# Kernel optimization log

Hardware: AMD Instinct MI355X
Metric: run time of the kernel (lower is better)

## Reference

```python
import jax, jax.numpy as jnp
from jax import lax
import numpy as np

B, T, D, U, K = 32, 1000, 512, 5, 3  # batch, frames, idim, upsample_times, conv kernel (l_order+r_order+1)
THRESHOLD = 1.0
TAIL = 0.45


def setup_inputs() -> dict:
    key = jax.random.key(0)
    ks = jax.random.split(key, 6)
    return {
        "encoder_out": jax.random.normal(ks[0], (B, T, D), jnp.float32),
        "mask": jnp.ones((B, 1, T), jnp.float32),
        "conv_w": jax.random.normal(ks[1], (D, D, K), jnp.float32) * 0.02,  # torch Conv1d [out,in,k]
        "conv_b": jnp.zeros((D,), jnp.float32),
        "up_w": jax.random.normal(ks[2], (D, D, U), jnp.float32) * 0.02,    # torch ConvTranspose1d [in,out,k]
        "up_b": jnp.zeros((D,), jnp.float32),
        "w1": jax.random.normal(ks[3], (D,), jnp.float32) * 0.05,           # cif_output Linear(D,1)
        "b1": jnp.zeros((), jnp.float32),
        "w2": jax.random.normal(ks[4], (D,), jnp.float32) * 0.05,           # cif_output2 Linear(D,1)
        "b2": jnp.zeros((), jnp.float32),
    }


def _cif(hidden, alphas, threshold):
    # hidden: [B, Tt, D], alphas: [B, Tt]
    Bb, Tt, Dd = hidden.shape

    def step(carry, inp):
        integrate, frame = carry
        alpha, h_t = inp  # [B], [B, D]
        dist_completion = 1.0 - integrate
        integrate = integrate + alpha
        fires_t = integrate
        fire = integrate >= threshold
        integrate = jnp.where(fire, integrate - 1.0, integrate)
        cur = jnp.where(fire, dist_completion, alpha)
        frame_out = frame + cur[:, None] * h_t
        frame = jnp.where(fire[:, None], (alpha - cur)[:, None] * h_t, frame_out)
        return (integrate, frame), (fires_t, frame_out)

    init = (jnp.zeros((Bb,), hidden.dtype), jnp.zeros((Bb, Dd), hidden.dtype))
    _, (fires, frames) = lax.scan(step, init, (alphas.T, jnp.swapaxes(hidden, 0, 1)))
    fires = fires.T                      # [B, Tt]
    frames = jnp.swapaxes(frames, 0, 1)  # [B, Tt, D]

    fire_mask = fires >= threshold

    def gather_b(frames_b, mask_b):
        pos = jnp.cumsum(mask_b.astype(jnp.int32)) - 1
        pos = jnp.where(mask_b, pos, Tt)  # non-fires -> out of range, dropped
        return jnp.zeros((Tt, Dd), frames_b.dtype).at[pos].set(frames_b, mode='drop')

    acoustic = jax.vmap(gather_b)(frames, fire_mask)  # [B, Tt, D] zero-padded
    return acoustic, fires


def reference(encoder_out, mask, conv_w, conv_b, up_w, up_b, w1, b1, w2, b2):
    Bb, Tt, Dd = encoder_out.shape
    context = jnp.swapaxes(encoder_out, 1, 2)           # [B, D, T]
    queries = jnp.pad(context, ((0, 0), (0, 0), (1, 1)))  # ConstantPad1d((1,1))
    conv = lax.conv_general_dilated(queries, conv_w, (1,), 'VALID',
                                    dimension_numbers=('NCH', 'OIH', 'NCH'))
    output = jax.nn.relu(conv + conv_b[None, :, None])  # [B, D, T]

    # ConvTranspose1d(stride=kernel=U, pad=0): non-overlapping -> einsum
    out2 = jnp.einsum('bit,ioj->btjo', output, up_w).reshape(Bb, Tt * U, Dd) + up_b  # [B, T*U, D]
    alphas2 = jax.nn.relu(jax.nn.sigmoid(out2 @ w2 + b2) * 1.0 - 0.0)  # smooth_factor2=1, noise_threshold2=0
    mask2 = jnp.swapaxes(jnp.broadcast_to(mask, (Bb, U, Tt)), 1, 2).reshape(Bb, Tt * U)
    alphas2 = alphas2 * mask2
    token_num2 = alphas2.sum(-1)

    h1 = jnp.swapaxes(output, 1, 2)  # [B, T, D]
    alphas = jax.nn.relu(jax.nn.sigmoid(h1 @ w1 + b1) * 1.0 - 0.0)  # smooth_factor=1, noise_threshold=0
    maskT = jnp.swapaxes(mask, 1, 2)[..., 0]  # [B, T]
    alphas = alphas * maskT

    # tail_process_fn (tail_threshold=0.45, mask given)
    zeros_t = jnp.zeros((Bb, 1), alphas.dtype)
    ones_t = jnp.ones((Bb, 1), alphas.dtype)
    mask_1 = jnp.concatenate([maskT, zeros_t], axis=1)
    mask_2 = jnp.concatenate([ones_t, maskT], axis=1)
    tail_add = (mask_2 - mask_1) * TAIL
    alphas_t = jnp.concatenate([alphas, zeros_t], axis=1) + tail_add  # [B, T+1]
    hidden = jnp.concatenate([encoder_out, jnp.zeros((Bb, 1, Dd), encoder_out.dtype)], axis=1)
    token_num = jnp.floor(alphas_t.sum(-1))

    acoustic_embeds, cif_peak = _cif(hidden, alphas_t, THRESHOLD)
    return acoustic_embeds, token_num, alphas_t, cif_peak, token_num2
```

## Files before the change

### kernel.cpp

```cpp
#include <hip/hip_runtime.h>
#include <math.h>

#define TB 32
#define TT 1000
#define TD 512
#define TU 5
#define TT1 1001

#define OFF_ACC  0
#define OFF_TOKN 16400384
#define OFF_ALPH 16400416
#define OFF_PEAK 16432448
#define OFF_TOK2 16464480

typedef _Float16 half8 __attribute__((ext_vector_type(8)));
typedef _Float16 half2t __attribute__((ext_vector_type(2)));
typedef float float4t __attribute__((ext_vector_type(4)));

typedef __attribute__((address_space(3))) uint32_t lds_u32_t;
typedef __attribute__((address_space(1))) const uint32_t g_u32_t;
#define GLOAD_LDS(gp, lp) __builtin_amdgcn_global_load_lds((g_u32_t*)(gp), (lds_u32_t*)(lp), 16, 0, 0)

#define BSTR 72
#define ASTR 200
#define EROWS 1032

#define WS_ARAW1 0
#define WS_ARAW2 32000
#define WS_VMAT  192000
#define WS_C2    194560
#define WS_WA    194564
#define WS_WB    226596
#define WS_FIRE  258628
#define WS_NF    290660
#define WS_ENCS_BYTES 1163264ull
#define WS_CWS_BYTES  (WS_ENCS_BYTES + 76059648ull)
#define WS_NEED_BYTES (WS_CWS_BYTES + 3276800ull)

__global__ __launch_bounds__(256) void kzero(float* araw1, float* araw2, float* tok2) {
    int idx = blockIdx.x * 256 + threadIdx.x;
    int stride = gridDim.x * 256;
    for (int i = idx; i < TB * TT; i += stride) araw1[i] = 0.f;
    for (int i = idx; i < TB * TT * TU; i += stride) araw2[i] = 0.f;
    if (idx < TB) tok2[idx] = 0.f;
}

__global__ __launch_bounds__(256) void kc2(const float* __restrict__ up_b, const float* __restrict__ w2,
                                           const float* __restrict__ b2, float* __restrict__ c2out) {
    int tid = threadIdx.x;
    float p = 0.f;
    for (int o = tid; o < TD; o += 256) p += up_b[o] * w2[o];
#pragma unroll
    for (int m = 1; m < 64; m <<= 1) p += __shfl_xor(p, m);
    __shared__ float wsum[4];
    if ((tid & 63) == 0) wsum[tid >> 6] = p;
    __syncthreads();
    if (tid == 0) c2out[0] = b2[0] + wsum[0] + wsum[1] + wsum[2] + wsum[3];
}

__global__ __launch_bounds__(64) void kv(const float* __restrict__ up_w, const float* __restrict__ w2,
                                         float* __restrict__ vmat) {
    int i = blockIdx.x, lane = threadIdx.x;
    float s0 = 0, s1 = 0, s2 = 0, s3 = 0, s4 = 0;
    for (int o = lane; o < TD; o += 64) {
        float w = w2[o];
        const float* p = up_w + (size_t)i * (TD * TU) + o * TU;
        s0 += p[0] * w; s1 += p[1] * w; s2 += p[2] * w; s3 += p[3] * w; s4 += p[4] * w;
    }
#pragma unroll
    for (int m = 1; m < 64; m <<= 1) {
        s0 += __shfl_xor(s0, m); s1 += __shfl_xor(s1, m); s2 += __shfl_xor(s2, m);
        s3 += __shfl_xor(s3, m); s4 += __shfl_xor(s4, m);
    }
    if (lane == 0) {
        float* d = vmat + i * TU;
        d[0] = s0; d[1] = s1; d[2] = s2; d[3] = s3; d[4] = s4;
    }
}

__global__ __launch_bounds__(256) void ksplitE(const float* __restrict__ enc, _Float16* __restrict__ encs) {
    int t = blockIdx.x, b = blockIdx.y, tid = threadIdx.x;
    int c = tid * 2;
    const float* p = &enc[((size_t)b * TT + t) * TD + c];
    float x0 = p[0], x1 = p[1];
    _Float16 h0 = (_Float16)x0, h1 = (_Float16)x1;
    _Float16 l0 = (_Float16)(x0 - (float)h0), l1 = (_Float16)(x1 - (float)h1);
    int ic = c >> 5, pos = c & 31;
    size_t base = ((size_t)(b * 16 + ic) * EROWS + 1 + t) * BSTR + pos;
    encs[base] = h0; encs[base + 1] = h1;
    encs[base + 32] = l0; encs[base + 33] = l1;
}

__global__ __launch_bounds__(256) void kpad(_Float16* __restrict__ encs) {
    uint32_t* p = (uint32_t*)encs;
    int idx = blockIdx.x * 256 + threadIdx.x;
    int stride = gridDim.x * 256;
    const int total = 512 * 32 * 36;
    for (int u = idx; u < total; u += stride) {
        int bic = u / (32 * 36);
        int r = (u / 36) % 32;
        int w = u % 36;
        int row = (r == 0) ? 0 : 1000 + r;
        p[((size_t)bic * EROWS + row) * 36 + w] = 0u;
    }
}

__global__ __launch_bounds__(64) void ksplitW(const float* __restrict__ cw, _Float16* __restrict__ cws) {
    int o = blockIdx.x, lane = threadIdx.x;
    for (int u = lane; u < 16 * 32 * 3; u += 64) {
        int tap = u % 3, pos = (u / 3) % 32, ic = u / 96;
        float x = cw[((size_t)o * TD + ic * 32 + pos) * 3 + tap];
        _Float16 h = (_Float16)x;
        _Float16 l = (_Float16)(x - (float)h);
        size_t base = (((size_t)(o >> 5) * 16 + ic) * 32 + (o & 31)) * ASTR + tap * 64;
        cws[base + pos] = h;
        cws[base + 32 + pos] = l;
    }
}

__global__ __launch_bounds__(256, 2) void kconvMD(const _Float16* __restrict__ encs,
                                                  const _Float16* __restrict__ cws,
                                                  const float* __restrict__ cb, const float* __restrict__ w1,
                                                  const float* __restrict__ vmat,
                                                  float* __restrict__ araw1, float* __restrict__ araw2) {
    __shared__ _Float16 sB[258 * BSTR];
    __shared__ _Float16 sA[64 * ASTR];

    const int tid = threadIdx.x;
    const int t0 = blockIdx.x * 256;
    const int oc = blockIdx.y;
    const int b = blockIdx.z;
    const int o0 = oc * 64;
    const int wv = tid >> 6, lane = tid & 63;
    const int q = lane >> 4, l15 = lane & 15;

    float4t acc[4][4];
#pragma unroll
    for (int i = 0; i < 4; ++i)
#pragma unroll
        for (int j = 0; j < 4; ++j) acc[i][j] = (float4t){0.f, 0.f, 0.f, 0.f};

    for (int ic = 0; ic < 16; ++ic) {
        __syncthreads();
        const _Float16* gB = encs + ((size_t)(b * 16 + ic) * EROWS + t0) * BSTR;
        for (int c = tid; c < 2322; c += 256) GLOAD_LDS(gB + c * 8, &sB[c * 8]);
        const _Float16* gA0 = cws + ((size_t)((oc * 2 + 0) * 16 + ic) * 32) * ASTR;
        const _Float16* gA1 = cws + ((size_t)((oc * 2 + 1) * 16 + ic) * 32) * ASTR;
        for (int c = tid; c < 800; c += 256) GLOAD_LDS(gA0 + c * 8, &sA[c * 8]);
        for (int c = tid; c < 800; c += 256) GLOAD_LDS(gA1 + c * 8, &sA[6400 + c * 8]);
        __syncthreads();
#pragma unroll
        for (int tap = 0; tap < 3; ++tap) {
            half8 Bh[4], Bl[4];
#pragma unroll
            for (int tt = 0; tt < 4; ++tt) {
                int s = wv * 64 + tt * 16 + l15 + tap;
                Bh[tt] = *(const half8*)&sB[s * BSTR + q * 8];
                Bl[tt] = *(const half8*)&sB[s * BSTR + 32 + q * 8];
            }
#pragma unroll
            for (int ot = 0; ot < 4; ++ot) {
                const int orow = ot * 16 + l15;
                half8 Ah = *(const half8*)&sA[orow * ASTR + tap * 64 + q * 8];
                half8 Al = *(const half8*)&sA[orow * ASTR + tap * 64 + 32 + q * 8];
#pragma unroll
                for (int tt = 0; tt < 4; ++tt) {
                    acc[ot][tt] = __builtin_amdgcn_mfma_f32_16x16x32_f16(Ah, Bh[tt], acc[ot][tt], 0, 0, 0);
                    acc[ot][tt] = __builtin_amdgcn_mfma_f32_16x16x32_f16(Ah, Bl[tt], acc[ot][tt], 0, 0, 0);
                    acc[ot][tt] = __builtin_amdgcn_mfma_f32_16x16x32_f16(Al, Bh[tt], acc[ot][tt], 0, 0, 0);
                }
            }
        }
    }

#pragma unroll
    for (int tt = 0; tt < 4; ++tt) {
        int t = t0 + wv * 64 + tt * 16 + l15;
        float s1 = 0.f, sa = 0.f, sb = 0.f, sc = 0.f, sd = 0.f, se = 0.f;
#pragma unroll
        for (int ot = 0; ot < 4; ++ot) {
#pragma unroll
            for (int r = 0; r < 4; ++r) {
                int o = o0 + ot * 16 + q * 4 + r;
                float rv = fmaxf(acc[ot][tt][r] + cb[o], 0.f);
                s1 = fmaf(w1[o], rv, s1);
                const float* vp = &vmat[o * 5];
                sa = fmaf(vp[0], rv, sa); sb = fmaf(vp[1], rv, sb);
                sc = fmaf(vp[2], rv, sc); sd = fmaf(vp[3], rv, sd);
                se = fmaf(vp[4], rv, se);
            }
        }
        s1 += __shfl_xor(s1, 16); sa += __shfl_xor(sa, 16); sb += __shfl_xor(sb, 16);
        sc += __shfl_xor(sc, 16); sd += __shfl_xor(sd, 16); se += __shfl_xor(se, 16);
        s1 += __shfl_xor(s1, 32); sa += __shfl_xor(sa, 32); sb += __shfl_xor(sb, 32);
        sc += __shfl_xor(sc, 32); sd += __shfl_xor(sd, 32); se += __shfl_xor(se, 32);
        if (q == 0 && t < TT) {
            atomicAdd(&araw1[b * TT + t], s1);
            float* p2 = &araw2[(b * TT + t) * 5];
            atomicAdd(p2 + 0, sa); atomicAdd(p2 + 1, sb); atomicAdd(p2 + 2, sc);
            atomicAdd(p2 + 3, sd); atomicAdd(p2 + 4, se);
        }
    }
}

__global__ __launch_bounds__(256, 3) void kconvM(const float* __restrict__ enc, const float* __restrict__ cw,
                                                 const float* __restrict__ cb, const float* __restrict__ w1,
                                                 const float* __restrict__ vmat,
                                                 float* __restrict__ araw1, float* __restrict__ araw2) {
    __shared__ _Float16 sB[258 * BSTR];
    __shared__ _Float16 sA[32 * ASTR];

    const int tid = threadIdx.x;
    const int t0 = blockIdx.x * 256;
    const int o0 = blockIdx.y * 32;
    const int b = blockIdx.z;
    const int wv = tid >> 6, lane = tid & 63;
    const int q = lane >> 4, l15 = lane & 15;

    float4t acc[2][4];
#pragma unroll
    for (int i = 0; i < 2; ++i)
#pragma unroll
        for (int j = 0; j < 4; ++j) acc[i][j] = (float4t){0.f, 0.f, 0.f, 0.f};

    for (int i0 = 0; i0 < TD; i0 += 32) {
        __syncthreads();
        for (int u = tid; u < 258 * 16; u += 256) {
            int s = u >> 4, ii2 = (u & 15) << 1;
            int t = t0 - 1 + s;
            float x0 = 0.f, x1 = 0.f;
            if (t >= 0 && t < TT) {
                const float* p = &enc[((size_t)b * TT + t) * TD + i0 + ii2];
                x0 = p[0]; x1 = p[1];
            }
            _Float16 h0 = (_Float16)x0, h1 = (_Float16)x1;
            _Float16 l0 = (_Float16)(x0 - (float)h0), l1 = (_Float16)(x1 - (float)h1);
            half2t hh; hh[0] = h0; hh[1] = h1;
            half2t ll; ll[0] = l0; ll[1] = l1;
            *(half2t*)&sB[s * BSTR + ii2] = hh;
            *(half2t*)&sB[s * BSTR + 32 + ii2] = ll;
        }
        for (int u = tid; u < 32 * 16; u += 256) {
            int o = u >> 4, ii2 = (u & 15) << 1;
            const float* p = &cw[((size_t)(o0 + o) * TD + i0 + ii2) * 3];
#pragma unroll
            for (int k = 0; k < 3; ++k) {
                float x0 = p[k], x1 = p[3 + k];
                _Float16 h0 = (_Float16)x0, h1 = (_Float16)x1;
                _Float16 l0 = (_Float16)(x0 - (float)h0), l1 = (_Float16)(x1 - (float)h1);
                half2t hh; hh[0] = h0; hh[1] = h1;
                half2t ll; ll[0] = l0; ll[1] = l1;
                *(half2t*)&sA[o * ASTR + k * 64 + ii2] = hh;
                *(half2t*)&sA[o * ASTR + k * 64 + 32 + ii2] = ll;
            }
        }
        __syncthreads();
#pragma unroll
        for (int tap = 0; tap < 3; ++tap) {
            half8 Bh[4], Bl[4];
#pragma unroll
            for (int tt = 0; tt < 4; ++tt) {
                int s = wv * 64 + tt * 16 + l15 + tap;
                Bh[tt] = *(const half8*)&sB[s * BSTR + q * 8];
                Bl[tt] = *(const half8*)&sB[s * BSTR + 32 + q * 8];
            }
#pragma unroll
            for (int ot = 0; ot < 2; ++ot) {
                const int orow = ot * 16 + l15;
                half8 Ah = *(const half8*)&sA[orow * ASTR + tap * 64 + q * 8];
                half8 Al = *(const half8*)&sA[orow * ASTR + tap * 64 + 32 + q * 8];
#pragma unroll
                for (int tt = 0; tt < 4; ++tt) {
                    acc[ot][tt] = __builtin_amdgcn_mfma_f32_16x16x32_f16(Ah, Bh[tt], acc[ot][tt], 0, 0, 0);
                    acc[ot][tt] = __builtin_amdgcn_mfma_f32_16x16x32_f16(Ah, Bl[tt], acc[ot][tt], 0, 0, 0);
                    acc[ot][tt] = __builtin_amdgcn_mfma_f32_16x16x32_f16(Al, Bh[tt], acc[ot][tt], 0, 0, 0);
                }
            }
        }
    }

#pragma unroll
    for (int tt = 0; tt < 4; ++tt) {
        int t = t0 + wv * 64 + tt * 16 + l15;
        float s1 = 0.f, sa = 0.f, sb = 0.f, sc = 0.f, sd = 0.f, se = 0.f;
#pragma unroll
        for (int ot = 0; ot < 2; ++ot) {
#pragma unroll
            for (int r = 0; r < 4; ++r) {
                int o = o0 + ot * 16 + q * 4 + r;
                float rv = fmaxf(acc[ot][tt][r] + cb[o], 0.f);
                s1 = fmaf(w1[o], rv, s1);
                const float* vp = &vmat[o * 5];
                sa = fmaf(vp[0], rv, sa); sb = fmaf(vp[1], rv, sb);
                sc = fmaf(vp[2], rv, sc); sd = fmaf(vp[3], rv, sd);
                se = fmaf(vp[4], rv, se);
            }
        }
        s1 += __shfl_xor(s1, 16); sa += __shfl_xor(sa, 16); sb += __shfl_xor(sb, 16);
        sc += __shfl_xor(sc, 16); sd += __shfl_xor(sd, 16); se += __shfl_xor(se, 16);
        s1 += __shfl_xor(s1, 32); sa += __shfl_xor(sa, 32); sb += __shfl_xor(sb, 32);
        sc += __shfl_xor(sc, 32); sd += __shfl_xor(sd, 32); se += __shfl_xor(se, 32);
        if (q == 0 && t < TT) {
            atomicAdd(&araw1[b * TT + t], s1);
            float* p2 = &araw2[(b * TT + t) * 5];
            atomicAdd(p2 + 0, sa); atomicAdd(p2 + 1, sb); atomicAdd(p2 + 2, sc);
            atomicAdd(p2 + 3, sd); atomicAdd(p2 + 4, se);
        }
    }
}

__global__ __launch_bounds__(256) void kalpha(const float* __restrict__ araw1, const float* __restrict__ araw2,
                                              const float* __restrict__ mask, const float* __restrict__ b1,
                                              const float* __restrict__ c2,
                                              float* __restrict__ alphas_t, float* __restrict__ tok2) {
    int b = blockIdx.y;
    int t = blockIdx.x * 256 + threadIdx.x;
    float sum5 = 0.f;
    if (t < TT) {
        float mk = mask[b * TT + t];
        float a1 = araw1[b * TT + t] + b1[0];
        float alpha = mk / (1.f + expf(-a1));
        float mprev = (t == 0) ? 1.f : mask[b * TT + t - 1];
        float tail = (mprev - mk) * 0.45f;
        alphas_t[b * TT1 + t] = alpha + tail;
        float cc = c2[0];
        float x0 = araw2[(b * TT + t) * 5 + 0] + cc;
        float x1 = araw2[(b * TT + t) * 5 + 1] + cc;
        float x2 = araw2[(b * TT + t) * 5 + 2] + cc;
        float x3 = araw2[(b * TT + t) * 5 + 3] + cc;
        float x4 = araw2[(b * TT + t) * 5 + 4] + cc;
        sum5 = mk / (1.f + expf(-x0)) + mk / (1.f + expf(-x1)) + mk / (1.f + expf(-x2))
             + mk / (1.f + expf(-x3)) + mk / (1.f + expf(-x4));
    } else if (t == TT) {
        alphas_t[b * TT1 + TT] = mask[b * TT + TT - 1] * 0.45f;
    }
#pragma unroll
    for (int m = 1; m < 64; m <<= 1) sum5 += __shfl_xor(sum5, m);
    if ((threadIdx.x & 63) == 0) atomicAdd(&tok2[b], sum5);
}

#define STEP(j, aj) { \
    float dist = 1.f - integ; \
    integ += (aj); \
    sp[tq + (j)] = integ; \
    bool fire = integ >= 1.f; \
    float cur = fire ? dist : (aj); \
    swa[tq + (j)] = cur; \
    swb[tq + (j)] = fire ? ((aj) - cur) : 0.f; \
    if (fire) { sf[F++] = tq + (j); integ -= 1.f; } \
    Ssum += (aj); }

__global__ __launch_bounds__(64) void kscan(const float* __restrict__ alphas_t,
                                            float* __restrict__ cif_peak, float* __restrict__ token_num,
                                            float* __restrict__ wA, float* __restrict__ wB,
                                            int* __restrict__ fire_time, int* __restrict__ n_fires) {
    __shared__ float sa[TT1 + 7], sp[TT1], swa[TT1], swb[TT1];
    __shared__ int sf[TT1];
    __shared__ int sFs;
    int b = blockIdx.x, lane = threadIdx.x;
    for (int t = lane; t < TT1 + 7; t += 64) sa[t] = (t < TT1) ? alphas_t[b * TT1 + t] : 0.f;
    __syncthreads();
    if (lane == 0) {
        float integ = 0.f, Ssum = 0.f;
        int F = 0;
        for (int tq = 0; tq < TT1 - 1; tq += 8) {
            float a0 = sa[tq], a1 = sa[tq + 1], a2 = sa[tq + 2], a3 = sa[tq + 3];
            float a4 = sa[tq + 4], a5 = sa[tq + 5], a6 = sa[tq + 6], a7 = sa[tq + 7];
            STEP(0, a0) STEP(1, a1) STEP(2, a2) STEP(3, a3)
            STEP(4, a4) STEP(5, a5) STEP(6, a6) STEP(7, a7)
        }
        { int tq = TT1 - 1; float a0 = sa[tq]; STEP(0, a0) }
        token_num[b] = floorf(Ssum);
        n_fires[b] = F;
        sFs = F;
    }
    __syncthreads();
    int F = sFs;
    for (int t = lane; t < TT1; t += 64) {
        cif_peak[b * TT1 + t] = sp[t];
        wA[b * TT1 + t] = swa[t];
        wB[b * TT1 + t] = swb[t];
        if (t < F) fire_time[b * TT1 + t] = sf[t];
    }
}

__global__ __launch_bounds__(128) void kgather(const float* __restrict__ enc,
                                               const float* __restrict__ wA, const float* __restrict__ wB,
                                               const int* __restrict__ fire_time, const int* __restrict__ n_fires,
                                               float* __restrict__ acoustic) {
    int k = blockIdx.x, b = blockIdx.y;
    int d4 = threadIdx.x;
    float ox = 0.f, oy = 0.f, oz = 0.f, ow = 0.f;
    int nf = n_fires[b];
    if (k < nf) {
        int end = fire_time[b * TT1 + k];
        int start = (k > 0) ? fire_time[b * TT1 + k - 1] : 0;
        for (int t = start; t <= end; ++t) {
            if (t >= TT) continue;
            float w = (k > 0 && t == start) ? wB[b * TT1 + t] : wA[b * TT1 + t];
            float4 h = ((const float4*)(enc + ((size_t)b * TT + t) * TD))[d4];
            ox += w * h.x; oy += w * h.y; oz += w * h.z; ow += w * h.w;
        }
    }
    float4 o4; o4.x = ox; o4.y = oy; o4.z = oz; o4.w = ow;
    ((float4*)(acoustic + ((size_t)b * TT1 + k) * TD))[d4] = o4;
}

extern "C" void kernel_launch(void* const* d_in, const int* in_sizes, int n_in,
                              void* d_out, int out_size, void* d_ws, size_t ws_size,
                              hipStream_t stream) {
    (void)in_sizes; (void)n_in; (void)out_size;
    const float* enc = (const float*)d_in[0];
    const float* mask = (const float*)d_in[1];
    const float* cw = (const float*)d_in[2];
    const float* cb = (const float*)d_in[3];
    const float* upw = (const float*)d_in[4];
    const float* upb = (const float*)d_in[5];
    const float* w1 = (const float*)d_in[6];
    const float* b1 = (const float*)d_in[7];
    const float* w2 = (const float*)d_in[8];
    const float* b2 = (const float*)d_in[9];

    float* out = (float*)d_out;
    float* acoustic = out + OFF_ACC;
    float* token_num = out + OFF_TOKN;
    float* alphas_t = out + OFF_ALPH;
    float* cif_peak = out + OFF_PEAK;
    float* tok2 = out + OFF_TOK2;

    float* ws = (float*)d_ws;
    float* araw1 = ws + WS_ARAW1;
    float* araw2 = ws + WS_ARAW2;
    float* vmat = ws + WS_VMAT;
    float* c2 = ws + WS_C2;
    float* wA = ws + WS_WA;
    float* wB = ws + WS_WB;
    int* fire_time = (int*)(ws + WS_FIRE);
    int* n_fires = (int*)(ws + WS_NF);
    _Float16* encs = (_Float16*)((char*)d_ws + WS_ENCS_BYTES);
    _Float16* cws = (_Float16*)((char*)d_ws + WS_CWS_BYTES);

    const bool bigws = (ws_size >= WS_NEED_BYTES);

    hipLaunchKernelGGL(kzero, dim3(256), dim3(256), 0, stream, araw1, araw2, tok2);
    hipLaunchKernelGGL(kc2, dim3(1), dim3(256), 0, stream, upb, w2, b2, c2);
    hipLaunchKernelGGL(kv, dim3(TD), dim3(64), 0, stream, upw, w2, vmat);
    if (bigws) {
        hipLaunchKernelGGL(kpad, dim3(1024), dim3(256), 0, stream, encs);
        hipLaunchKernelGGL(ksplitE, dim3(TT, TB), dim3(256), 0, stream, enc, encs);
        hipLaunchKernelGGL(ksplitW, dim3(TD), dim3(64), 0, stream, cw, cws);
        hipLaunchKernelGGL(kconvMD, dim3(4, 8, TB), dim3(256), 0, stream, encs, cws, cb, w1, vmat, araw1, araw2);
    } else {
        hipLaunchKernelGGL(kconvM, dim3(4, 16, TB), dim3(256), 0, stream, enc, cw, cb, w1, vmat, araw1, araw2);
    }
    hipLaunchKernelGGL(kalpha, dim3(4, TB), dim3(256), 0, stream, araw1, araw2, mask, b1, c2, alphas_t, tok2);
    hipLaunchKernelGGL(kscan, dim3(TB), dim3(64), 0, stream, alphas_t, cif_peak, token_num, wA, wB, fire_time, n_fires);
    hipLaunchKernelGGL(kgather, dim3(TT1, TB), dim3(128), 0, stream, enc, wA, wB, fire_time, n_fires, acoustic);
}
```

Before: 394.4 us.

## Double-buffer conv LDS tiles to overlap global loads with MFMA compute

Rewrites the kconvMD input-channel loop to ping-pong between two dynamic-LDS buffers. The next tile is issued through global_load_lds while MFMAs run on the current one, with a single waitcnt+barrier per stage. This is meant to hide load latency that was previously serialized behind two syncthreads per iteration. LDS use roughly doubles, so launch bounds drop to one block per SIMD group, which cuts occupancy. The MFMA issue order is also regrouped by split component.

```diff
diff --git a/kernel.cpp b/kernel.cpp
--- a/kernel.cpp
+++ b/kernel.cpp
@@ -24,6 +24,10 @@
 #define BSTR 72
 #define ASTR 200
 #define EROWS 1032
+
+#define SB_HALVES 18576
+#define BUF_HALVES 31376
+#define SMEM_BYTES (2 * BUF_HALVES * 2)
 
 #define WS_ARAW1 0
 #define WS_ARAW2 32000
@@ -37,6 +41,13 @@
 #define WS_CWS_BYTES  (WS_ENCS_BYTES + 76059648ull)
 #define WS_NEED_BYTES (WS_CWS_BYTES + 3276800ull)
 
+#define PIPE_BARRIER() do { \
+    asm volatile("s_waitcnt vmcnt(0)" ::: "memory"); \
+    __builtin_amdgcn_sched_barrier(0); \
+    __builtin_amdgcn_s_barrier(); \
+    __builtin_amdgcn_sched_barrier(0); \
+} while (0)
+
 __global__ __launch_bounds__(256) void kzero(float* araw1, float* araw2, float* tok2) {
     int idx = blockIdx.x * 256 + threadIdx.x;
     int stride = gridDim.x * 256;
@@ -118,13 +129,57 @@
     }
 }
 
-__global__ __launch_bounds__(256, 2) void kconvMD(const _Float16* __restrict__ encs,
+__device__ __forceinline__ void stage_tile(const _Float16* __restrict__ encs,
+                                           const _Float16* __restrict__ cws,
+                                           int b, int oc, int ic, int t0, int tid,
+                                           _Float16* sB, _Float16* sA) {
+    const _Float16* gB = encs + ((size_t)(b * 16 + ic) * EROWS + t0) * BSTR;
+    for (int c = tid; c < 2322; c += 256) GLOAD_LDS(gB + c * 8, &sB[c * 8]);
+    const _Float16* gA0 = cws + ((size_t)((oc * 2 + 0) * 16 + ic) * 32) * ASTR;
+    const _Float16* gA1 = cws + ((size_t)((oc * 2 + 1) * 16 + ic) * 32) * ASTR;
+    for (int c = tid; c < 800; c += 256) GLOAD_LDS(gA0 + c * 8, &sA[c * 8]);
+    for (int c = tid; c < 800; c += 256) GLOAD_LDS(gA1 + c * 8, &sA[6400 + c * 8]);
+}
+
+__device__ __forceinline__ void compute_tile(const _Float16* sB, const _Float16* sA,
+                                             int wv, int q, int l15, float4t (&acc)[4][4]) {
+#pragma unroll
+    for (int tap = 0; tap < 3; ++tap) {
+        half8 Bh[4], Bl[4];
+#pragma unroll
+        for (int tt = 0; tt < 4; ++tt) {
+            int s = wv * 64 + tt * 16 + l15 + tap;
+            Bh[tt] = *(const half8*)&sB[s * BSTR + q * 8];
+            Bl[tt] = *(const half8*)&sB[s * BSTR + 32 + q * 8];
+        }
+#pragma unroll
+        for (int ot = 0; ot < 4; ++ot) {
+            const int orow = ot * 16 + l15;
+            half8 Ah = *(const half8*)&sA[orow * ASTR + tap * 64 + q * 8];
+            half8 Al = *(const half8*)&sA[orow * ASTR + tap * 64 + 32 + q * 8];
+#pragma unroll
+            for (int tt = 0; tt < 4; ++tt)
+                acc[ot][tt] = __builtin_amdgcn_mfma_f32_16x16x32_f16(Ah, Bh[tt], acc[ot][tt], 0, 0, 0);
+#pragma unroll
+            for (int tt = 0; tt < 4; ++tt)
+                acc[ot][tt] = __builtin_amdgcn_mfma_f32_16x16x32_f16(Ah, Bl[tt], acc[ot][tt], 0, 0, 0);
+#pragma unroll
+            for (int tt = 0; tt < 4; ++tt)
+                acc[ot][tt] = __builtin_amdgcn_mfma_f32_16x16x32_f16(Al, Bh[tt], acc[ot][tt], 0, 0, 0);
+        }
+    }
+}
+
+__global__ __launch_bounds__(256, 1) void kconvMD(const _Float16* __restrict__ encs,
                                                   const _Float16* __restrict__ cws,
                                                   const float* __restrict__ cb, const float* __restrict__ w1,
                                                   const float* __restrict__ vmat,
                                                   float* __restrict__ araw1, float* __restrict__ araw2) {
-    __shared__ _Float16 sB[258 * BSTR];
-    __shared__ _Float16 sA[64 * ASTR];
+    extern __shared__ _Float16 smem[];
+    _Float16* sB0 = smem;
+    _Float16* sA0 = smem + SB_HALVES;
+    _Float16* sB1 = smem + BUF_HALVES;
+    _Float16* sA1 = smem + BUF_HALVES + SB_HALVES;
 
     const int tid = threadIdx.x;
     const int t0 = blockIdx.x * 256;
@@ -140,37 +195,17 @@
 #pragma unroll
         for (int j = 0; j < 4; ++j) acc[i][j] = (float4t){0.f, 0.f, 0.f, 0.f};
 
-    for (int ic = 0; ic < 16; ++ic) {
-        __syncthreads();
-        const _Float16* gB = encs + ((size_t)(b * 16 + ic) * EROWS + t0) * BSTR;
-        for (int c = tid; c < 2322; c += 256) GLOAD_LDS(gB + c * 8, &sB[c * 8]);
-        const _Float16* gA0 = cws + ((size_t)((oc * 2 + 0) * 16 + ic) * 32) * ASTR;
-        const _Float16* gA1 = cws + ((size_t)((oc * 2 + 1) * 16 + ic) * 32) * ASTR;
-        for (int c = tid; c < 800; c += 256) GLOAD_LDS(gA0 + c * 8, &sA[c * 8]);
-        for (int c = tid; c < 800; c += 256) GLOAD_LDS(gA1 + c * 8, &sA[6400 + c * 8]);
-        __syncthreads();
-#pragma unroll
-        for (int tap = 0; tap < 3; ++tap) {
-            half8 Bh[4], Bl[4];
-#pragma unroll
-            for (int tt = 0; tt < 4; ++tt) {
-                int s = wv * 64 + tt * 16 + l15 + tap;
-                Bh[tt] = *(const half8*)&sB[s * BSTR + q * 8];
-                Bl[tt] = *(const half8*)&sB[s * BSTR + 32 + q * 8];
-            }
-#pragma unroll
-            for (int ot = 0; ot < 4; ++ot) {
-                const int orow = ot * 16 + l15;
-                half8 Ah = *(const half8*)&sA[orow * ASTR + tap * 64 + q * 8];
-                half8 Al = *(const half8*)&sA[orow * ASTR + tap * 64 + 32 + q * 8];
-#pragma unroll
-                for (int tt = 0; tt < 4; ++tt) {
-                    acc[ot][tt] = __builtin_amdgcn_mfma_f32_16x16x32_f16(Ah, Bh[tt], acc[ot][tt], 0, 0, 0);
-                    acc[ot][tt] = __builtin_amdgcn_mfma_f32_16x16x32_f16(Ah, Bl[tt], acc[ot][tt], 0, 0, 0);
-                    acc[ot][tt] = __builtin_amdgcn_mfma_f32_16x16x32_f16(Al, Bh[tt], acc[ot][tt], 0, 0, 0);
-                }
-            }
-        }
+    stage_tile(encs, cws, b, oc, 0, t0, tid, sB0, sA0);
+    PIPE_BARRIER();
+
+#pragma unroll 1
+    for (int ic = 0; ic < 16; ic += 2) {
+        stage_tile(encs, cws, b, oc, ic + 1, t0, tid, sB1, sA1);
+        compute_tile(sB0, sA0, wv, q, l15, acc);
+        PIPE_BARRIER();
+        if (ic + 2 < 16) stage_tile(encs, cws, b, oc, ic + 2, t0, tid, sB0, sA0);
+        compute_tile(sB1, sA1, wv, q, l15, acc);
+        PIPE_BARRIER();
     }
 
 #pragma unroll
@@ -442,6 +477,13 @@
 
     const bool bigws = (ws_size >= WS_NEED_BYTES);
 
+    static bool attr_set = false;
+    if (!attr_set) {
+        hipFuncSetAttribute(reinterpret_cast<const void*>(&kconvMD),
+                            hipFuncAttributeMaxDynamicSharedMemorySize, SMEM_BYTES);
+        attr_set = true;
+    }
+
     hipLaunchKernelGGL(kzero, dim3(256), dim3(256), 0, stream, araw1, araw2, tok2);
     hipLaunchKernelGGL(kc2, dim3(1), dim3(256), 0, stream, upb, w2, b2, c2);
     hipLaunchKernelGGL(kv, dim3(TD), dim3(64), 0, stream, upw, w2, vmat);
@@ -449,7 +491,8 @@
         hipLaunchKernelGGL(kpad, dim3(1024), dim3(256), 0, stream, encs);
         hipLaunchKernelGGL(ksplitE, dim3(TT, TB), dim3(256), 0, stream, enc, encs);
         hipLaunchKernelGGL(ksplitW, dim3(TD), dim3(64), 0, stream, cw, cws);
-        hipLaunchKernelGGL(kconvMD, dim3(4, 8, TB), dim3(256), 0, stream, encs, cws, cb, w1, vmat, araw1, araw2);
+        hipLaunchKernelGGL(kconvMD, dim3(4, 8, TB), dim3(256), SMEM_BYTES, stream,
+                           encs, cws, cb, w1, vmat, araw1, araw2);
     } else {
         hipLaunchKernelGGL(kconvM, dim3(4, 16, TB), dim3(256), 0, stream, enc, cw, cb, w1, vmat, araw1, araw2);
     }
```

After: 439.0 us. +11.3%, slower.
